# Kernel tuning notes

Hardware: AMD Instinct MI355X
Metric: run time of the kernel (lower is better)

Reference implementation:

```python
import jax, jax.numpy as jnp
import numpy as np

# Static module config (from Encoder's CropConv layers)
B, CIN, COUT, H, W = 32, 256, 256, 64, 64
K, STRIDE, PAD, DIL = 3, 2, 1, 1
OVERLAP, CENTER = 0, 4


def _build_crop_mask(in_h, out_h, out_w, center_size, overlap):
    """Faithful replica of CropConv's python-loop mask construction,
    including python-slice clamping to L = out_h*out_w."""
    L = out_h * out_w
    crop_start = (in_h - in_h // center_size) // 2 - overlap
    start_idx = in_h * crop_start + crop_start
    crop_size = in_h // center_size + overlap * 2
    not_cropped = crop_start * 2

    def seg_len(a, b):
        # length of python slice [a:b] on an array of length L
        return max(0, min(b, L) - min(a, L))

    segs = []
    for i in range(crop_size):
        if i == 0:
            segs.append(np.ones(seg_len(0, start_idx), bool))
        if i == crop_size - 1:
            segs.append(np.zeros(seg_len(start_idx, start_idx + crop_size), bool))
            segs.append(np.ones(seg_len(start_idx + crop_size, in_h * in_h), bool))
            break
        segs.append(np.zeros(seg_len(start_idx, start_idx + crop_size), bool))
        segs.append(np.ones(seg_len(start_idx + crop_size, start_idx + not_cropped), bool))
        start_idx += in_h
    mask = np.concatenate(segs)
    assert mask.shape[0] == L, (mask.shape[0], L)
    return mask.reshape(out_h, out_w)


def setup_inputs() -> dict:
    key = jax.random.key(0)
    kx, kw = jax.random.split(key)
    x = jax.random.normal(kx, (B, CIN, H, W), dtype=jnp.float32)
    # kaiming_normal(mode='fan_out', nonlinearity='relu'): std = sqrt(2 / (COUT*K*K))
    std = np.sqrt(2.0 / (COUT * K * K)).astype(np.float32)
    weight = jax.random.normal(kw, (COUT, CIN, K, K), dtype=jnp.float32) * std
    return {"x": x, "weight": weight}


def reference(x, weight):
    out_h = (H - K + 2 * PAD) // STRIDE + 1
    out_w = (W - K + 2 * PAD) // STRIDE + 1
    # unfold + matmul == standard convolution; use the efficient fused form
    out = jax.lax.conv_general_dilated(
        x, weight,
        window_strides=(STRIDE, STRIDE),
        padding=[(PAD, PAD), (PAD, PAD)],
        rhs_dilation=(DIL, DIL),
        dimension_numbers=("NCHW", "OIHW", "NCHW"))  # [B, COUT, out_h, out_w]
    mask = jnp.asarray(_build_crop_mask(H, out_h, out_w, CENTER, OVERLAP))
    return jnp.where(mask[None, None, :, :], out, jnp.float32(0.0))
```

## Files before the change

kernel.cpp:

```cpp
#include <hip/hip_runtime.h>


#define CIN  256
#define H_   64
#define W_   64
#define OH   32
#define OW   32
#define HW   4096

typedef _Float16 f16;
typedef _Float16 half8 __attribute__((ext_vector_type(8)));
typedef _Float16 half4 __attribute__((ext_vector_type(4)));
typedef float    f32x4 __attribute__((ext_vector_type(4)));
typedef float    floatx16 __attribute__((ext_vector_type(16)));

typedef const __attribute__((address_space(1))) void g_void;
typedef __attribute__((address_space(3))) void l_void;

__global__ __launch_bounds__(256) void repack_w_kernel(const float* __restrict__ w,
                                                       f16* __restrict__ rp) {
  int o = blockIdx.x * 256 + threadIdx.x;
  int co_l = o & 127;
  int t2   = o >> 7;
  int h    = t2 & 1;
  int t3   = t2 >> 1;
  int khw  = t3 % 9;
  int t4   = t3 / 9;
  int cc   = t4 & 15;
  int co_t = t4 >> 4;
  int co  = co_t * 128 + co_l;
  int ci0 = cc * 16 + h * 8;
  half8 v;
#pragma unroll
  for (int j = 0; j < 8; ++j) v[j] = (f16)w[(co * CIN + ci0 + j) * 9 + khw];
  *(half8*)(rp + (size_t)o * 8) = v;
}

__global__ __launch_bounds__(256, 2) void conv_mfma_kernel(
    const float* __restrict__ x, const f16* __restrict__ rp,
    float* __restrict__ out) {
  __shared__ f16 ws[9 * 2 * 128 * 8];
  __shared__ f16 xs[9 * 2 * 2 * 33 * 8];

  const int t    = threadIdx.x;
  const int lane = t & 63;
  const int wave = t >> 6;
  const int h    = lane >> 5;
  const int ml   = lane & 31;
  const int wm   = wave >> 1;
  const int wn   = wave & 1;

  const int blk  = blockIdx.x;
  const int co_t = blk & 1;
  const int ohg  = (blk >> 1) & 7;
  const int b    = blk >> 4;
  const int oh0  = ohg * 4;
  const int ih0  = 2 * oh0 - 1;

  const float* xb  = x  + (size_t)b * CIN * HW;
  const f16*   rpb = rp + (size_t)co_t * (16 * 18432);

  if (t < 18) {
    int r = t >> 1, hh = t & 1;
    half8 z = {};
    *(half8*)&xs[(((r * 2 + 1) * 2 + hh) * 33 + 0) * 8] = z;
  }

  floatx16 acc[2][2];
#pragma unroll
  for (int mi = 0; mi < 2; ++mi)
#pragma unroll
    for (int nj = 0; nj < 2; ++nj)
#pragma unroll
      for (int i = 0; i < 16; ++i) acc[mi][nj][i] = 0.f;

  for (int cc = 0; cc < 16; ++cc) {
    __syncthreads();
    {
      const char* src = (const char*)rpb + (size_t)cc * 36864 + wave * 9216 + lane * 16;
      char* dst = (char*)ws + wave * 9216 + lane * 16;
#pragma unroll
      for (int i = 0; i < 9; ++i)
        __builtin_amdgcn_global_load_lds((g_void*)(src + i * 1024),
                                         (l_void*)(dst + i * 1024), 16, 0, 0);
    }
#pragma unroll
    for (int it = 0; it < 3; ++it) {
      int u = t + it * 256;
      if (u < 576) {
        int iwq = u & 15;
        int rg  = u >> 4;
        int r   = rg % 9;
        int g   = rg / 9;
        int ih  = ih0 + r;
        int ihc = ih < 0 ? 0 : ih;
        const float* bp = xb + (size_t)(cc * 16 + g * 4) * HW + (size_t)ihc * W_ + iwq * 4;
        f32x4 v0 = *(const f32x4*)(bp);
        f32x4 v1 = *(const f32x4*)(bp + HW);
        f32x4 v2 = *(const f32x4*)(bp + 2 * HW);
        f32x4 v3 = *(const f32x4*)(bp + 3 * HW);
        if (ih < 0) {
          f32x4 z = {0.f, 0.f, 0.f, 0.f};
          v0 = z; v1 = z; v2 = z; v3 = z;
        }
        const int hh  = g >> 1;
        const int sub = (g & 1) * 4;
#pragma unroll
        for (int o = 0; o < 4; ++o) {
          int iw  = iwq * 4 + o;
          int p   = iw & 1;
          int idx = (iw + p) >> 1;
          half4 d;
          d[0] = (f16)v0[o];
          d[1] = (f16)v1[o];
          d[2] = (f16)v2[o];
          d[3] = (f16)v3[o];
          *(half4*)&xs[(((r * 2 + p) * 2 + hh) * 33 + idx) * 8 + sub] = d;
        }
      }
    }
    __syncthreads();

#pragma unroll
    for (int kh = 0; kh < 3; ++kh) {
#pragma unroll
      for (int kw = 0; kw < 3; ++kw) {
        const int khw = kh * 3 + kw;
        half8 a0 = *(const half8*)&ws[((khw * 2 + h) * 128 + wm * 64 + ml) * 8];
        half8 a1 = *(const half8*)&ws[((khw * 2 + h) * 128 + wm * 64 + 32 + ml) * 8];
        const int pp = (kw & 1) ^ 1;
        const int ix = ml + (kw >> 1);
#pragma unroll
        for (int nj = 0; nj < 2; ++nj) {
          const int r = 2 * (wn * 2 + nj) + kh;
          half8 bf = *(const half8*)&xs[(((r * 2 + pp) * 2 + h) * 33 + ix) * 8];
          acc[0][nj] = __builtin_amdgcn_mfma_f32_32x32x16_f16(a0, bf, acc[0][nj], 0, 0, 0);
          acc[1][nj] = __builtin_amdgcn_mfma_f32_32x32x16_f16(a1, bf, acc[1][nj], 0, 0, 0);
        }
      }
    }
  }

  float* ob = out + ((size_t)b * 256 + co_t * 128 + wm * 64) * (OH * OW);
  const int rb4 = h * 4;
#pragma unroll
  for (int mi = 0; mi < 2; ++mi) {
#pragma unroll
    for (int nj = 0; nj < 2; ++nj) {
      const int oh = oh0 + wn * 2 + nj;
#pragma unroll
      for (int r = 0; r < 16; ++r) {
        const int row = mi * 32 + (r & 3) + 8 * (r >> 2) + rb4;
        ob[(size_t)row * (OH * OW) + oh * OW + ml] = acc[mi][nj][r];
      }
    }
  }
}

extern "C" void kernel_launch(void* const* d_in, const int* in_sizes, int n_in,
                              void* d_out, int out_size, void* d_ws, size_t ws_size,
                              hipStream_t stream) {
  const float* x = (const float*)d_in[0];
  const float* w = (const float*)d_in[1];
  float* out = (float*)d_out;
  f16* rp = (f16*)d_ws;

  repack_w_kernel<<<288, 256, 0, stream>>>(w, rp);
  conv_mfma_kernel<<<512, 256, 0, stream>>>(x, rp, out);
}
```

Before: 245.8 us.

## Halve output-channel tile to 64 per block and double grid for occupancy

Each block now computes 64 output channels instead of 128, so each wave holds two accumulators instead of four, LDS weight storage is halved, and launch bounds rise to 4 blocks per CU. The grid doubles to 1024 blocks, with the channel quarter taken from the high block-index bits so blocks sharing the same input tile are spread apart. The weight repack layout is changed to match. The aim is more occupancy and latency hiding, at the cost of converting and loading each input tile into LDS four times rather than twice, with less MFMA work per byte loaded.

```diff
diff --git a/kernel.cpp b/kernel.cpp
--- a/kernel.cpp
+++ b/kernel.cpp
@@ -20,15 +20,15 @@
 __global__ __launch_bounds__(256) void repack_w_kernel(const float* __restrict__ w,
                                                        f16* __restrict__ rp) {
   int o = blockIdx.x * 256 + threadIdx.x;
-  int co_l = o & 127;
-  int t2   = o >> 7;
+  int co_l = o & 63;
+  int t2   = o >> 6;
   int h    = t2 & 1;
   int t3   = t2 >> 1;
   int khw  = t3 % 9;
   int t4   = t3 / 9;
   int cc   = t4 & 15;
-  int co_t = t4 >> 4;
-  int co  = co_t * 128 + co_l;
+  int co_q = t4 >> 4;
+  int co  = co_q * 64 + co_l;
   int ci0 = cc * 16 + h * 8;
   half8 v;
 #pragma unroll
@@ -36,10 +36,10 @@
   *(half8*)(rp + (size_t)o * 8) = v;
 }
 
-__global__ __launch_bounds__(256, 2) void conv_mfma_kernel(
+__global__ __launch_bounds__(256, 4) void conv_mfma_kernel(
     const float* __restrict__ x, const f16* __restrict__ rp,
     float* __restrict__ out) {
-  __shared__ f16 ws[9 * 2 * 128 * 8];
+  __shared__ f16 ws[9 * 2 * 64 * 8];
   __shared__ f16 xs[9 * 2 * 2 * 33 * 8];
 
   const int t    = threadIdx.x;
@@ -51,14 +51,15 @@
   const int wn   = wave & 1;
 
   const int blk  = blockIdx.x;
-  const int co_t = blk & 1;
-  const int ohg  = (blk >> 1) & 7;
-  const int b    = blk >> 4;
+  const int co_q = blk >> 8;
+  const int g8   = blk & 255;
+  const int b    = g8 >> 3;
+  const int ohg  = g8 & 7;
   const int oh0  = ohg * 4;
   const int ih0  = 2 * oh0 - 1;
 
   const float* xb  = x  + (size_t)b * CIN * HW;
-  const f16*   rpb = rp + (size_t)co_t * (16 * 18432);
+  const f16*   rpq = rp + (size_t)co_q * (16 * 9216);
 
   if (t < 18) {
     int r = t >> 1, hh = t & 1;
@@ -66,23 +67,24 @@
     *(half8*)&xs[(((r * 2 + 1) * 2 + hh) * 33 + 0) * 8] = z;
   }
 
-  floatx16 acc[2][2];
+  floatx16 acc[2];
 #pragma unroll
-  for (int mi = 0; mi < 2; ++mi)
+  for (int nj = 0; nj < 2; ++nj)
 #pragma unroll
-    for (int nj = 0; nj < 2; ++nj)
-#pragma unroll
-      for (int i = 0; i < 16; ++i) acc[mi][nj][i] = 0.f;
+    for (int i = 0; i < 16; ++i) acc[nj][i] = 0.f;
 
   for (int cc = 0; cc < 16; ++cc) {
     __syncthreads();
     {
-      const char* src = (const char*)rpb + (size_t)cc * 36864 + wave * 9216 + lane * 16;
-      char* dst = (char*)ws + wave * 9216 + lane * 16;
+      const char* src = (const char*)rpq + (size_t)cc * 18432;
+      char* dst = (char*)ws;
 #pragma unroll
-      for (int i = 0; i < 9; ++i)
-        __builtin_amdgcn_global_load_lds((g_void*)(src + i * 1024),
-                                         (l_void*)(dst + i * 1024), 16, 0, 0);
+      for (int k = 0; k < 5; ++k) {
+        int u = t + k * 256;
+        if (u < 1152)
+          __builtin_amdgcn_global_load_lds((g_void*)(src + u * 16),
+                                           (l_void*)(dst + u * 16), 16, 0, 0);
+      }
     }
 #pragma unroll
     for (int it = 0; it < 3; ++it) {
@@ -126,33 +128,28 @@
 #pragma unroll
       for (int kw = 0; kw < 3; ++kw) {
         const int khw = kh * 3 + kw;
-        half8 a0 = *(const half8*)&ws[((khw * 2 + h) * 128 + wm * 64 + ml) * 8];
-        half8 a1 = *(const half8*)&ws[((khw * 2 + h) * 128 + wm * 64 + 32 + ml) * 8];
+        half8 a0 = *(const half8*)&ws[((khw * 2 + h) * 64 + wm * 32 + ml) * 8];
         const int pp = (kw & 1) ^ 1;
         const int ix = ml + (kw >> 1);
 #pragma unroll
         for (int nj = 0; nj < 2; ++nj) {
           const int r = 2 * (wn * 2 + nj) + kh;
           half8 bf = *(const half8*)&xs[(((r * 2 + pp) * 2 + h) * 33 + ix) * 8];
-          acc[0][nj] = __builtin_amdgcn_mfma_f32_32x32x16_f16(a0, bf, acc[0][nj], 0, 0, 0);
-          acc[1][nj] = __builtin_amdgcn_mfma_f32_32x32x16_f16(a1, bf, acc[1][nj], 0, 0, 0);
+          acc[nj] = __builtin_amdgcn_mfma_f32_32x32x16_f16(a0, bf, acc[nj], 0, 0, 0);
         }
       }
     }
   }
 
-  float* ob = out + ((size_t)b * 256 + co_t * 128 + wm * 64) * (OH * OW);
+  float* ob = out + ((size_t)b * 256 + co_q * 64 + wm * 32) * (OH * OW);
   const int rb4 = h * 4;
 #pragma unroll
-  for (int mi = 0; mi < 2; ++mi) {
+  for (int nj = 0; nj < 2; ++nj) {
+    const int oh = oh0 + wn * 2 + nj;
 #pragma unroll
-    for (int nj = 0; nj < 2; ++nj) {
-      const int oh = oh0 + wn * 2 + nj;
-#pragma unroll
-      for (int r = 0; r < 16; ++r) {
-        const int row = mi * 32 + (r & 3) + 8 * (r >> 2) + rb4;
-        ob[(size_t)row * (OH * OW) + oh * OW + ml] = acc[mi][nj][r];
-      }
+    for (int r = 0; r < 16; ++r) {
+      const int row = (r & 3) + 8 * (r >> 2) + rb4;
+      ob[(size_t)row * (OH * OW) + oh * OW + ml] = acc[nj][r];
     }
   }
 }
@@ -166,5 +163,5 @@
   f16* rp = (f16*)d_ws;
 
   repack_w_kernel<<<288, 256, 0, stream>>>(w, rp);
-  conv_mfma_kernel<<<512, 256, 0, stream>>>(x, rp, out);
+  conv_mfma_kernel<<<1024, 256, 0, stream>>>(x, rp, out);
 }
```

After: 247.8 us. No clear change (+0.8%).
